# Performance work log

Hardware: AMD Instinct MI355X
Metric: run time of the kernel (lower is better)

The kernel has to match this reference:

```python
import jax, jax.numpy as jnp
import numpy as np

NUM_GROUPS = 32
EPS = 1e-6

def group_norm(x, gamma, beta):
    # x: (b, c, h, w)
    b, c, h, w = x.shape
    xg = x.reshape(b, NUM_GROUPS, c // NUM_GROUPS, h, w)
    mean = xg.mean(axis=(2, 3, 4), keepdims=True)
    var = xg.var(axis=(2, 3, 4), keepdims=True)
    xn = ((xg - mean) * jax.lax.rsqrt(var + EPS)).reshape(b, c, h, w)
    return xn * gamma[None, :, None, None] + beta[None, :, None, None]

def conv1x1(x, W, bias):
    # W: (out_c, in_c); 1x1 conv == channel matmul
    return jnp.einsum('oc,bchw->bohw', W, x) + bias[None, :, None, None]

def setup_inputs() -> dict:
    key = jax.random.key(0)
    ks = jax.random.split(key, 11)
    C = 512
    x = jax.random.normal(ks[0], (4, C, 64, 64), dtype=jnp.float32)
    s = 1.0 / np.sqrt(C)
    d = {
        'x': x,
        'gamma': jnp.ones((C,), jnp.float32),
        'beta': jnp.zeros((C,), jnp.float32),
        'Wq': jax.random.normal(ks[1], (C, C), jnp.float32) * s,
        'bq': jax.random.normal(ks[2], (C,), jnp.float32) * 0.01,
        'Wk': jax.random.normal(ks[3], (C, C), jnp.float32) * s,
        'bk': jax.random.normal(ks[4], (C,), jnp.float32) * 0.01,
        'Wv': jax.random.normal(ks[5], (C, C), jnp.float32) * s,
        'bv': jax.random.normal(ks[6], (C,), jnp.float32) * 0.01,
        'Wp': jax.random.normal(ks[7], (C, C), jnp.float32) * s,
        'bp': jax.random.normal(ks[8], (C,), jnp.float32) * 0.01,
    }
    return d

def reference(x, gamma, beta, Wq, bq, Wk, bk, Wv, bv, Wp, bp):
    b, c, h, w = x.shape
    hn = group_norm(x, gamma, beta)
    q = conv1x1(hn, Wq, bq).reshape(b, c, h * w)  # (b,c,n)
    k = conv1x1(hn, Wk, bk).reshape(b, c, h * w)
    v = conv1x1(hn, Wv, bv).reshape(b, c, h * w)
    scale = jnp.asarray(c, x.dtype) ** -0.5
    # scores[b,m,n] = sum_c q[b,c,m] * k[b,c,n]
    scores = jnp.einsum('bcm,bcn->bmn', q, k) * scale
    attn = jax.nn.softmax(scores, axis=2)  # softmax over key positions n
    # h_[b,c,m] = sum_n v[b,c,n] * attn[b,m,n]
    out = jnp.einsum('bcn,bmn->bcm', v, attn).reshape(b, c, h, w)
    return x + conv1x1(out, Wp, bp)
```

## Files before the change

### kernel.cpp

```cpp
#include <hip/hip_runtime.h>
#include <math.h>


#define BATCH 4
#define CH    512
#define NPOS  4096
#define NGRP  32
#define GSIZE (16 * NPOS)
#define WSZ   262144

typedef __attribute__((ext_vector_type(8))) short bf16x8;
typedef __attribute__((ext_vector_type(4))) float f32x4;

__device__ __forceinline__ ushort f2b(float x) {
    uint u = __float_as_uint(x);
    u += 0x7fff + ((u >> 16) & 1);
    return (ushort)(u >> 16);
}

__device__ __forceinline__ void gld16(void* lds, const void* g) {
    __builtin_amdgcn_global_load_lds(
        (const __attribute__((address_space(1))) void*)g,
        (__attribute__((address_space(3))) void*)lds, 16, 0, 0);
}

__global__ __launch_bounds__(256) void gn_stats_k(const float* __restrict__ x,
                                                  float* __restrict__ stats) {
    int bg = blockIdx.x;
    const float4* xp = reinterpret_cast<const float4*>(x + (size_t)bg * GSIZE);
    float s1 = 0.f, s2 = 0.f;
    for (int i = threadIdx.x; i < GSIZE / 4; i += 256) {
        float4 v = xp[i];
        s1 += v.x + v.y + v.z + v.w;
        s2 += v.x * v.x + v.y * v.y + v.z * v.z + v.w * v.w;
    }
    for (int off = 32; off > 0; off >>= 1) {
        s1 += __shfl_down(s1, off);
        s2 += __shfl_down(s2, off);
    }
    __shared__ float r1[4], r2[4];
    int wid = threadIdx.x >> 6;
    if ((threadIdx.x & 63) == 0) { r1[wid] = s1; r2[wid] = s2; }
    __syncthreads();
    if (threadIdx.x == 0) {
        float t1 = r1[0] + r1[1] + r1[2] + r1[3];
        float t2 = r2[0] + r2[1] + r2[2] + r2[3];
        float mean = t1 / (float)GSIZE;
        float var  = t2 / (float)GSIZE - mean * mean;
        stats[bg]       = mean;
        stats[128 + bg] = rsqrtf(var + 1e-6f);
    }
}

__global__ __launch_bounds__(256) void wcvt_k(
    const float* __restrict__ Wq, const float* __restrict__ Wk,
    const float* __restrict__ Wv, const float* __restrict__ Wp,
    ushort* __restrict__ W4) {
    int id = blockIdx.x;
    int sel = id >> 7, blk = id & 127;
    const float* src = sel == 0 ? Wq : (sel == 1 ? Wk : (sel == 2 ? Wv : Wp));
    const float4* s4 = (const float4*)(src + (size_t)blk * 2048);
    ushort4* d4 = (ushort4*)(W4 + (size_t)sel * WSZ + (size_t)blk * 2048);
    for (int i = threadIdx.x; i < 512; i += 256) {
        float4 v = s4[i];
        d4[i] = make_ushort4(f2b(v.x), f2b(v.y), f2b(v.z), f2b(v.w));
    }
}

__global__ __launch_bounds__(256) void hnT_k(
    const float* __restrict__ x, const float* __restrict__ gamma,
    const float* __restrict__ beta, const float* __restrict__ stats,
    ushort* __restrict__ hnT) {
    int bm = blockIdx.x * 64, c0 = blockIdx.y * 64, b = blockIdx.z;
    __shared__ ushort Ls[64][65];
    int t = threadIdx.x, tx = t & 15, ty = t >> 4;
    const float* xb = x + ((size_t)b * CH + c0) * NPOS + bm;
#pragma unroll
    for (int it = 0; it < 4; ++it) {
        int cc = ty + it * 16;
        int ch = c0 + cc;
        int bg = b * NGRP + (ch >> 4);
        float ga = stats[128 + bg] * gamma[ch];
        float be = beta[ch] - stats[bg] * ga;
        float4 v = *(const float4*)(xb + (size_t)cc * NPOS + tx * 4);
        Ls[cc][tx * 4 + 0] = f2b(v.x * ga + be);
        Ls[cc][tx * 4 + 1] = f2b(v.y * ga + be);
        Ls[cc][tx * 4 + 2] = f2b(v.z * ga + be);
        Ls[cc][tx * 4 + 3] = f2b(v.w * ga + be);
    }
    __syncthreads();
#pragma unroll
    for (int it = 0; it < 4; ++it) {
        int mm = ty + it * 16;
        ushort4 o;
        o.x = Ls[tx * 4 + 0][mm];
        o.y = Ls[tx * 4 + 1][mm];
        o.z = Ls[tx * 4 + 2][mm];
        o.w = Ls[tx * 4 + 3][mm];
        *(ushort4*)(hnT + ((size_t)(b * NPOS) + bm + mm) * CH + c0 + tx * 4) = o;
    }
}

__global__ __launch_bounds__(256) void qkv3_k(
    const ushort* __restrict__ hnT, const ushort* __restrict__ W4,
    const float* __restrict__ bq, const float* __restrict__ bk,
    const float* __restrict__ bv,
    ushort* __restrict__ qT, ushort* __restrict__ kT, ushort* __restrict__ vB) {
    int bm = blockIdx.x * 64, bo = blockIdx.y * 64, b = blockIdx.z;
    int t = threadIdx.x, l = t & 63, w = t >> 6;
    int wr = w & 1, wc = w >> 1;
    int lr = l & 15, lg = l >> 4;

    const ushort* ha  = hnT + ((size_t)(b * NPOS) + bm + wr * 32 + lr) * CH + lg * 8;
    const ushort* wqp = W4 + (size_t)(bo + wc * 32 + lr) * CH + lg * 8;
    const ushort* wkp = wqp + WSZ;
    const ushort* wvp = wkp + WSZ;

    f32x4 aq[2][2], ak[2][2], av[2][2];
#pragma unroll
    for (int i = 0; i < 2; ++i)
#pragma unroll
        for (int j = 0; j < 2; ++j) {
            aq[i][j] = (f32x4){0.f, 0.f, 0.f, 0.f};
            ak[i][j] = (f32x4){0.f, 0.f, 0.f, 0.f};
            av[i][j] = (f32x4){0.f, 0.f, 0.f, 0.f};
        }
#pragma unroll
    for (int c0 = 0; c0 < CH; c0 += 32) {
        bf16x8 a0 = *(const bf16x8*)(ha + c0);
        bf16x8 a1 = *(const bf16x8*)(ha + 16 * CH + c0);
        bf16x8 q0 = *(const bf16x8*)(wqp + c0);
        bf16x8 q1 = *(const bf16x8*)(wqp + 16 * CH + c0);
        bf16x8 k0 = *(const bf16x8*)(wkp + c0);
        bf16x8 k1 = *(const bf16x8*)(wkp + 16 * CH + c0);
        bf16x8 v0 = *(const bf16x8*)(wvp + c0);
        bf16x8 v1 = *(const bf16x8*)(wvp + 16 * CH + c0);
        aq[0][0] = __builtin_amdgcn_mfma_f32_16x16x32_bf16(a0, q0, aq[0][0], 0, 0, 0);
        aq[0][1] = __builtin_amdgcn_mfma_f32_16x16x32_bf16(a0, q1, aq[0][1], 0, 0, 0);
        aq[1][0] = __builtin_amdgcn_mfma_f32_16x16x32_bf16(a1, q0, aq[1][0], 0, 0, 0);
        aq[1][1] = __builtin_amdgcn_mfma_f32_16x16x32_bf16(a1, q1, aq[1][1], 0, 0, 0);
        ak[0][0] = __builtin_amdgcn_mfma_f32_16x16x32_bf16(a0, k0, ak[0][0], 0, 0, 0);
        ak[0][1] = __builtin_amdgcn_mfma_f32_16x16x32_bf16(a0, k1, ak[0][1], 0, 0, 0);
        ak[1][0] = __builtin_amdgcn_mfma_f32_16x16x32_bf16(a1, k0, ak[1][0], 0, 0, 0);
        ak[1][1] = __builtin_amdgcn_mfma_f32_16x16x32_bf16(a1, k1, ak[1][1], 0, 0, 0);
        av[0][0] = __builtin_amdgcn_mfma_f32_16x16x32_bf16(v0, a0, av[0][0], 0, 0, 0);
        av[0][1] = __builtin_amdgcn_mfma_f32_16x16x32_bf16(v0, a1, av[0][1], 0, 0, 0);
        av[1][0] = __builtin_amdgcn_mfma_f32_16x16x32_bf16(v1, a0, av[1][0], 0, 0, 0);
        av[1][1] = __builtin_amdgcn_mfma_f32_16x16x32_bf16(v1, a1, av[1][1], 0, 0, 0);
    }
    const float sc = 0.044194173824159216f;
#pragma unroll
    for (int j = 0; j < 2; ++j) {
        int o = bo + wc * 32 + j * 16 + lr;
        float bqv = bq[o], bkv = bk[o];
#pragma unroll
        for (int i = 0; i < 2; ++i)
#pragma unroll
            for (int r = 0; r < 4; ++r) {
                int m = bm + wr * 32 + i * 16 + 4 * lg + r;
                size_t base = ((size_t)(b * NPOS) + m) * CH + o;
                qT[base] = f2b((aq[i][j][r] + bqv) * sc);
                kT[base] = f2b(ak[i][j][r] + bkv);
            }
    }
#pragma unroll
    for (int i = 0; i < 2; ++i)
#pragma unroll
        for (int r = 0; r < 4; ++r) {
            int o = bo + wc * 32 + i * 16 + 4 * lg + r;
            float bvv = bv[o];
#pragma unroll
            for (int j = 0; j < 2; ++j) {
                int m = bm + wr * 32 + j * 16 + lr;
                vB[((size_t)(b * CH) + o) * NPOS + m] = f2b(av[i][j][r] + bvv);
            }
        }
}

__global__ __launch_bounds__(512) __attribute__((amdgpu_waves_per_eu(2, 2)))
void attn_k(
    const ushort* __restrict__ qT, const ushort* __restrict__ kT,
    const ushort* __restrict__ vB, ushort* __restrict__ aoT) {
    __shared__ ushort Ks[2][32 * 512];
    __shared__ ushort Vs[2][512 * 32];
    __shared__ ushort P_lds[64 * 40];
    __shared__ float mpart[2][4][16];

    int id = blockIdx.x;
    int b  = (id & 7) >> 1;
    int mt = ((id >> 3) << 1) | (id & 1);
    int m0 = mt * 64;

    int t = threadIdx.x, l = t & 63, w = t >> 6;
    int mi = w & 3, ci = w >> 2;
    int lr = l & 15, lg = l >> 4;

    const ushort* kTb = kT + (size_t)b * NPOS * CH;
    const ushort* vBb = vB + (size_t)b * CH * NPOS;

    auto stageK = [&](int n0, ushort* kbuf) {
#pragma unroll
        for (int i = 0; i < 4; ++i) {
            int n = w * 4 + i;
            const ushort* g = kTb + (size_t)(n0 + n) * CH + (l ^ (n & 7)) * 8;
            gld16(&kbuf[n * 512], g);
        }
    };
    auto stageV = [&](int n0, ushort* vbuf) {
#pragma unroll
        for (int i = 0; i < 4; ++i) {
            int cb = w * 64 + i * 16;
            int c  = cb + (l >> 2);
            int sc = (l & 3) ^ ((c >> 1) & 3);
            const ushort* g = vBb + (size_t)c * NPOS + n0 + sc * 8;
            gld16(&vbuf[cb * 32], g);
        }
    };

    stageK(0, &Ks[0][0]);
    stageV(0, &Vs[0][0]);

    const ushort* qrow = qT + ((size_t)(b * NPOS + m0 + mi * 16 + lr)) * CH + lg * 8;
    bf16x8 qf[16];
#pragma unroll
    for (int ks = 0; ks < 16; ++ks) qf[ks] = *(const bf16x8*)(qrow + ks * 32);

    f32x4 acc[16];
#pragma unroll
    for (int i = 0; i < 16; ++i) acc[i] = (f32x4){0.f, 0.f, 0.f, 0.f};
    float m_run[4], lsum[4];
#pragma unroll
    for (int r = 0; r < 4; ++r) { m_run[r] = -1e30f; lsum[r] = 0.f; }

    int zk = lr & 7;
    for (int nt = 0; nt < 128; ++nt) {
        const ushort* ks_cur = &Ks[nt & 1][0];
        const ushort* vs_cur = &Vs[nt & 1][0];
        asm volatile("s_waitcnt vmcnt(0)" ::: "memory");
        __builtin_amdgcn_s_barrier();
        __builtin_amdgcn_sched_barrier(0);
        if (nt + 1 < 128) {
            stageK((nt + 1) * 32, &Ks[(nt + 1) & 1][0]);
            stageV((nt + 1) * 32, &Vs[(nt + 1) & 1][0]);
        }
        f32x4 sp0 = {0.f, 0.f, 0.f, 0.f}, sp1 = sp0, sp2 = sp0, sp3 = sp0;
        const ushort* krow = &ks_cur[(ci * 16 + lr) * 512];
#pragma unroll
        for (int ks = 0; ks < 16; ks += 4) {
            bf16x8 kf0 = *(const bf16x8*)(krow + (((ks + 0) * 4 + lg) ^ zk) * 8);
            bf16x8 kf1 = *(const bf16x8*)(krow + (((ks + 1) * 4 + lg) ^ zk) * 8);
            bf16x8 kf2 = *(const bf16x8*)(krow + (((ks + 2) * 4 + lg) ^ zk) * 8);
            bf16x8 kf3 = *(const bf16x8*)(krow + (((ks + 3) * 4 + lg) ^ zk) * 8);
            sp0 = __builtin_amdgcn_mfma_f32_16x16x32_bf16(qf[ks + 0], kf0, sp0, 0, 0, 0);
            sp1 = __builtin_amdgcn_mfma_f32_16x16x32_bf16(qf[ks + 1], kf1, sp1, 0, 0, 0);
            sp2 = __builtin_amdgcn_mfma_f32_16x16x32_bf16(qf[ks + 2], kf2, sp2, 0, 0, 0);
            sp3 = __builtin_amdgcn_mfma_f32_16x16x32_bf16(qf[ks + 3], kf3, sp3, 0, 0, 0);
        }
        f32x4 s = (sp0 + sp1) + (sp2 + sp3);
        float pm[4];
#pragma unroll
        for (int r = 0; r < 4; ++r) pm[r] = s[r];
#pragma unroll
        for (int off = 1; off < 16; off <<= 1)
#pragma unroll
            for (int r = 0; r < 4; ++r) pm[r] = fmaxf(pm[r], __shfl_xor(pm[r], off));
        if (lr == 0) {
#pragma unroll
            for (int r = 0; r < 4; ++r) mpart[ci][mi][4 * lg + r] = pm[r];
        }
        asm volatile("s_waitcnt lgkmcnt(0)" ::: "memory");
        __builtin_amdgcn_s_barrier();
        __builtin_amdgcn_sched_barrier(0);
        float mt2[4];
        float growth = -1e30f;
#pragma unroll
        for (int r = 0; r < 4; ++r) {
            int row = 4 * lg + r;
            mt2[r] = fmaxf(mpart[0][mi][row], mpart[1][mi][row]);
            growth = fmaxf(growth, mt2[r] - m_run[r]);
        }
        bool resc = !__all(growth <= 8.0f);
        if (resc) {
            float alpha[4];
#pragma unroll
            for (int r = 0; r < 4; ++r) {
                float mnew = fmaxf(m_run[r], mt2[r]);
                alpha[r] = __expf(m_run[r] - mnew);
                m_run[r] = mnew;
                lsum[r] *= alpha[r];
            }
#pragma unroll
            for (int cs = 0; cs < 16; ++cs) {
                acc[cs][0] *= alpha[0]; acc[cs][1] *= alpha[1];
                acc[cs][2] *= alpha[2]; acc[cs][3] *= alpha[3];
            }
        }
        float p[4];
#pragma unroll
        for (int r = 0; r < 4; ++r) {
            p[r] = __expf(s[r] - m_run[r]);
            lsum[r] += p[r];
        }
#pragma unroll
        for (int r = 0; r < 4; ++r)
            P_lds[(mi * 16 + 4 * lg + r) * 40 + ci * 16 + lr] = f2b(p[r]);
        asm volatile("s_waitcnt lgkmcnt(0)" ::: "memory");
        __builtin_amdgcn_s_barrier();
        __builtin_amdgcn_sched_barrier(0);
        bf16x8 pa = *(const bf16x8*)&P_lds[(mi * 16 + lr) * 40 + lg * 8];
#pragma unroll
        for (int cs = 0; cs < 16; ++cs) {
            int c = ci * 256 + cs * 16 + lr;
            bf16x8 vf = *(const bf16x8*)&vs_cur[c * 32 + ((lg ^ ((c >> 1) & 3)) * 8)];
            acc[cs] = __builtin_amdgcn_mfma_f32_16x16x32_bf16(pa, vf, acc[cs], 0, 0, 0);
        }
    }
    float ls[4];
#pragma unroll
    for (int r = 0; r < 4; ++r) ls[r] = lsum[r];
#pragma unroll
    for (int off = 1; off < 16; off <<= 1)
#pragma unroll
        for (int r = 0; r < 4; ++r) ls[r] += __shfl_xor(ls[r], off);
    if (lr == 0) {
#pragma unroll
        for (int r = 0; r < 4; ++r) mpart[ci][mi][4 * lg + r] = ls[r];
    }
    asm volatile("s_waitcnt lgkmcnt(0)" ::: "memory");
    __builtin_amdgcn_s_barrier();
    __builtin_amdgcn_sched_barrier(0);
    float inv[4];
#pragma unroll
    for (int r = 0; r < 4; ++r) {
        int row = 4 * lg + r;
        inv[r] = 1.0f / (mpart[0][mi][row] + mpart[1][mi][row]);
    }
#pragma unroll
    for (int cs = 0; cs < 16; ++cs)
#pragma unroll
        for (int r = 0; r < 4; ++r)
            aoT[((size_t)(b * NPOS + m0 + mi * 16 + 4 * lg + r)) * CH
                + ci * 256 + cs * 16 + lr] = f2b(acc[cs][r] * inv[r]);
}

__global__ __launch_bounds__(256) void proj_k(
    const ushort* __restrict__ aoT, const ushort* __restrict__ W4,
    const float* __restrict__ bp, const float* __restrict__ x,
    float* __restrict__ out) {
    int bm = blockIdx.x * 64, bo = blockIdx.y * 64, b = blockIdx.z;
    int t = threadIdx.x, l = t & 63, w = t >> 6;
    int orh = w & 1, mc = w >> 1;
    int lr = l & 15, lg = l >> 4;

    const ushort* wp = W4 + 3 * (size_t)WSZ + (size_t)(bo + orh * 32 + lr) * CH + lg * 8;
    const ushort* ab = aoT + ((size_t)(b * NPOS) + bm + mc * 32 + lr) * CH + lg * 8;

    f32x4 ac[2][2];
#pragma unroll
    for (int i = 0; i < 2; ++i)
#pragma unroll
        for (int j = 0; j < 2; ++j) ac[i][j] = (f32x4){0.f, 0.f, 0.f, 0.f};
#pragma unroll
    for (int c0 = 0; c0 < CH; c0 += 32) {
        bf16x8 w0 = *(const bf16x8*)(wp + c0);
        bf16x8 w1 = *(const bf16x8*)(wp + 16 * CH + c0);
        bf16x8 b0 = *(const bf16x8*)(ab + c0);
        bf16x8 b1 = *(const bf16x8*)(ab + 16 * CH + c0);
        ac[0][0] = __builtin_amdgcn_mfma_f32_16x16x32_bf16(w0, b0, ac[0][0], 0, 0, 0);
        ac[0][1] = __builtin_amdgcn_mfma_f32_16x16x32_bf16(w0, b1, ac[0][1], 0, 0, 0);
        ac[1][0] = __builtin_amdgcn_mfma_f32_16x16x32_bf16(w1, b0, ac[1][0], 0, 0, 0);
        ac[1][1] = __builtin_amdgcn_mfma_f32_16x16x32_bf16(w1, b1, ac[1][1], 0, 0, 0);
    }
#pragma unroll
    for (int i = 0; i < 2; ++i)
#pragma unroll
        for (int r = 0; r < 4; ++r) {
            int o = bo + orh * 32 + i * 16 + 4 * lg + r;
            float bpv = bp[o];
#pragma unroll
            for (int j = 0; j < 2; ++j) {
                int m = bm + mc * 32 + j * 16 + lr;
                size_t base = ((size_t)(b * CH) + o) * NPOS + m;
                out[base] = ac[i][j][r] + bpv + x[base];
            }
        }
}

extern "C" void kernel_launch(void* const* d_in, const int* in_sizes, int n_in,
                              void* d_out, int out_size, void* d_ws, size_t ws_size,
                              hipStream_t stream) {
    const float* x     = (const float*)d_in[0];
    const float* gamma = (const float*)d_in[1];
    const float* beta  = (const float*)d_in[2];
    const float* Wq    = (const float*)d_in[3];
    const float* bq    = (const float*)d_in[4];
    const float* Wk    = (const float*)d_in[5];
    const float* bk    = (const float*)d_in[6];
    const float* Wv    = (const float*)d_in[7];
    const float* bv    = (const float*)d_in[8];
    const float* Wp    = (const float*)d_in[9];
    const float* bp    = (const float*)d_in[10];
    float* out = (float*)d_out;

    const size_t SZ = (size_t)BATCH * CH * NPOS;
    const size_t need = (5 * SZ + 4 * WSZ) * 2 + 1024;
    if (ws_size < need) return;

    ushort* qT  = (ushort*)d_ws;
    ushort* kT  = qT + SZ;
    ushort* vb  = kT + SZ;
    ushort* hnT = vb + SZ;
    ushort* aoT = hnT + SZ;
    ushort* W4  = aoT + SZ;
    float*  stats = (float*)(W4 + 4 * (size_t)WSZ);

    gn_stats_k<<<128, 256, 0, stream>>>(x, stats);
    wcvt_k<<<512, 256, 0, stream>>>(Wq, Wk, Wv, Wp, W4);
    hnT_k<<<dim3(64, 8, 4), 256, 0, stream>>>(x, gamma, beta, stats, hnT);
    qkv3_k<<<dim3(64, 8, 4), 256, 0, stream>>>(hnT, W4, bq, bk, bv, qT, kT, vb);
    attn_k<<<dim3(256), 512, 0, stream>>>(qT, kT, vb, aoT);
    proj_k<<<dim3(64, 8, 4), 256, 0, stream>>>(aoT, W4, bp, x, out);
}
```

Before: 500.1 us.

## Widen attention KV tile to 64 and single-buffer K/V with staggered prefetch

The attention kernel now processes 64 key positions per iteration instead of 32, halving the number of loop iterations and barriers, and drops double buffering. K and V each get a single LDS buffer. V for the current tile is loaded at the start of the iteration, while K for the next tile is issued after the max-reduction barrier, using partial vmcnt waits. The V swizzle is changed to an 8-way XOR. The aim is to amortize the softmax/barrier overhead over more MFMA work while keeping LDS use similar, at the risk of exposing V load latency before the PV matmul.

```diff
diff --git a/kernel.cpp b/kernel.cpp
--- a/kernel.cpp
+++ b/kernel.cpp
@@ -8,6 +8,8 @@
 #define NGRP  32
 #define GSIZE (16 * NPOS)
 #define WSZ   262144
+#define KVB   64
+#define NT    64
 
 typedef __attribute__((ext_vector_type(8))) short bf16x8;
 typedef __attribute__((ext_vector_type(4))) float f32x4;
@@ -181,9 +183,9 @@
 void attn_k(
     const ushort* __restrict__ qT, const ushort* __restrict__ kT,
     const ushort* __restrict__ vB, ushort* __restrict__ aoT) {
-    __shared__ ushort Ks[2][32 * 512];
-    __shared__ ushort Vs[2][512 * 32];
-    __shared__ ushort P_lds[64 * 40];
+    __shared__ ushort Ks[KVB * 512];
+    __shared__ ushort Vs[512 * KVB];
+    __shared__ ushort P_lds[64 * 72];
     __shared__ float mpart[2][4][16];
 
     int id = blockIdx.x;
@@ -198,27 +200,26 @@
     const ushort* kTb = kT + (size_t)b * NPOS * CH;
     const ushort* vBb = vB + (size_t)b * CH * NPOS;
 
-    auto stageK = [&](int n0, ushort* kbuf) {
-#pragma unroll
-        for (int i = 0; i < 4; ++i) {
-            int n = w * 4 + i;
+    auto stageK = [&](int n0) {
+#pragma unroll
+        for (int i = 0; i < 8; ++i) {
+            int n = w * 8 + i;
             const ushort* g = kTb + (size_t)(n0 + n) * CH + (l ^ (n & 7)) * 8;
-            gld16(&kbuf[n * 512], g);
+            gld16(&Ks[n * 512], g);
         }
     };
-    auto stageV = [&](int n0, ushort* vbuf) {
-#pragma unroll
-        for (int i = 0; i < 4; ++i) {
-            int cb = w * 64 + i * 16;
-            int c  = cb + (l >> 2);
-            int sc = (l & 3) ^ ((c >> 1) & 3);
+    auto stageV = [&](int n0) {
+#pragma unroll
+        for (int i = 0; i < 8; ++i) {
+            int cb = w * 64 + i * 8;
+            int c  = cb + (l >> 3);
+            int sc = (l & 7) ^ (c & 7);
             const ushort* g = vBb + (size_t)c * NPOS + n0 + sc * 8;
-            gld16(&vbuf[cb * 32], g);
+            gld16(&Vs[cb * KVB], g);
         }
     };
 
-    stageK(0, &Ks[0][0]);
-    stageV(0, &Vs[0][0]);
+    stageK(0);
 
     const ushort* qrow = qT + ((size_t)(b * NPOS + m0 + mi * 16 + lr)) * CH + lg * 8;
     bf16x8 qf[16];
@@ -233,33 +234,31 @@
     for (int r = 0; r < 4; ++r) { m_run[r] = -1e30f; lsum[r] = 0.f; }
 
     int zk = lr & 7;
-    for (int nt = 0; nt < 128; ++nt) {
-        const ushort* ks_cur = &Ks[nt & 1][0];
-        const ushort* vs_cur = &Vs[nt & 1][0];
+    for (int nt = 0; nt < NT; ++nt) {
+        int n0 = nt * KVB;
         asm volatile("s_waitcnt vmcnt(0)" ::: "memory");
         __builtin_amdgcn_s_barrier();
         __builtin_amdgcn_sched_barrier(0);
-        if (nt + 1 < 128) {
-            stageK((nt + 1) * 32, &Ks[(nt + 1) & 1][0]);
-            stageV((nt + 1) * 32, &Vs[(nt + 1) & 1][0]);
-        }
-        f32x4 sp0 = {0.f, 0.f, 0.f, 0.f}, sp1 = sp0, sp2 = sp0, sp3 = sp0;
-        const ushort* krow = &ks_cur[(ci * 16 + lr) * 512];
-#pragma unroll
-        for (int ks = 0; ks < 16; ks += 4) {
-            bf16x8 kf0 = *(const bf16x8*)(krow + (((ks + 0) * 4 + lg) ^ zk) * 8);
-            bf16x8 kf1 = *(const bf16x8*)(krow + (((ks + 1) * 4 + lg) ^ zk) * 8);
-            bf16x8 kf2 = *(const bf16x8*)(krow + (((ks + 2) * 4 + lg) ^ zk) * 8);
-            bf16x8 kf3 = *(const bf16x8*)(krow + (((ks + 3) * 4 + lg) ^ zk) * 8);
-            sp0 = __builtin_amdgcn_mfma_f32_16x16x32_bf16(qf[ks + 0], kf0, sp0, 0, 0, 0);
-            sp1 = __builtin_amdgcn_mfma_f32_16x16x32_bf16(qf[ks + 1], kf1, sp1, 0, 0, 0);
-            sp2 = __builtin_amdgcn_mfma_f32_16x16x32_bf16(qf[ks + 2], kf2, sp2, 0, 0, 0);
-            sp3 = __builtin_amdgcn_mfma_f32_16x16x32_bf16(qf[ks + 3], kf3, sp3, 0, 0, 0);
-        }
-        f32x4 s = (sp0 + sp1) + (sp2 + sp3);
+        stageV(n0);
+        f32x4 s0a = {0.f, 0.f, 0.f, 0.f}, s0b = s0a, s1a = s0a, s1b = s0a;
+        const ushort* krow0 = &Ks[(ci * 32 + lr) * 512];
+        const ushort* krow1 = &Ks[(ci * 32 + 16 + lr) * 512];
+#pragma unroll
+        for (int ks = 0; ks < 16; ks += 2) {
+            bf16x8 k0a = *(const bf16x8*)(krow0 + (((ks + 0) * 4 + lg) ^ zk) * 8);
+            bf16x8 k0b = *(const bf16x8*)(krow0 + (((ks + 1) * 4 + lg) ^ zk) * 8);
+            bf16x8 k1a = *(const bf16x8*)(krow1 + (((ks + 0) * 4 + lg) ^ zk) * 8);
+            bf16x8 k1b = *(const bf16x8*)(krow1 + (((ks + 1) * 4 + lg) ^ zk) * 8);
+            s0a = __builtin_amdgcn_mfma_f32_16x16x32_bf16(qf[ks + 0], k0a, s0a, 0, 0, 0);
+            s0b = __builtin_amdgcn_mfma_f32_16x16x32_bf16(qf[ks + 1], k0b, s0b, 0, 0, 0);
+            s1a = __builtin_amdgcn_mfma_f32_16x16x32_bf16(qf[ks + 0], k1a, s1a, 0, 0, 0);
+            s1b = __builtin_amdgcn_mfma_f32_16x16x32_bf16(qf[ks + 1], k1b, s1b, 0, 0, 0);
+        }
+        f32x4 s0 = s0a + s0b;
+        f32x4 s1 = s1a + s1b;
         float pm[4];
 #pragma unroll
-        for (int r = 0; r < 4; ++r) pm[r] = s[r];
+        for (int r = 0; r < 4; ++r) pm[r] = fmaxf(s0[r], s1[r]);
 #pragma unroll
         for (int off = 1; off < 16; off <<= 1)
 #pragma unroll
@@ -271,6 +270,7 @@
         asm volatile("s_waitcnt lgkmcnt(0)" ::: "memory");
         __builtin_amdgcn_s_barrier();
         __builtin_amdgcn_sched_barrier(0);
+        if (nt + 1 < NT) stageK((nt + 1) * KVB);
         float mt2[4];
         float growth = -1e30f;
 #pragma unroll
@@ -295,24 +295,36 @@
                 acc[cs][2] *= alpha[2]; acc[cs][3] *= alpha[3];
             }
         }
-        float p[4];
+        float p0[4], p1[4];
 #pragma unroll
         for (int r = 0; r < 4; ++r) {
-            p[r] = __expf(s[r] - m_run[r]);
-            lsum[r] += p[r];
-        }
-#pragma unroll
-        for (int r = 0; r < 4; ++r)
-            P_lds[(mi * 16 + 4 * lg + r) * 40 + ci * 16 + lr] = f2b(p[r]);
+            p0[r] = __expf(s0[r] - m_run[r]);
+            p1[r] = __expf(s1[r] - m_run[r]);
+            lsum[r] += p0[r] + p1[r];
+        }
+#pragma unroll
+        for (int r = 0; r < 4; ++r) {
+            int row = mi * 16 + 4 * lg + r;
+            P_lds[row * 72 + ci * 32 + lr]      = f2b(p0[r]);
+            P_lds[row * 72 + ci * 32 + 16 + lr] = f2b(p1[r]);
+        }
+        if (nt + 1 < NT) {
+            asm volatile("s_waitcnt vmcnt(8)" ::: "memory");
+        } else {
+            asm volatile("s_waitcnt vmcnt(0)" ::: "memory");
+        }
         asm volatile("s_waitcnt lgkmcnt(0)" ::: "memory");
         __builtin_amdgcn_s_barrier();
         __builtin_amdgcn_sched_barrier(0);
-        bf16x8 pa = *(const bf16x8*)&P_lds[(mi * 16 + lr) * 40 + lg * 8];
+        bf16x8 pa0 = *(const bf16x8*)&P_lds[(mi * 16 + lr) * 72 + lg * 8];
+        bf16x8 pa1 = *(const bf16x8*)&P_lds[(mi * 16 + lr) * 72 + 32 + lg * 8];
 #pragma unroll
         for (int cs = 0; cs < 16; ++cs) {
             int c = ci * 256 + cs * 16 + lr;
-            bf16x8 vf = *(const bf16x8*)&vs_cur[c * 32 + ((lg ^ ((c >> 1) & 3)) * 8)];
-            acc[cs] = __builtin_amdgcn_mfma_f32_16x16x32_bf16(pa, vf, acc[cs], 0, 0, 0);
+            bf16x8 vf0 = *(const bf16x8*)&Vs[c * KVB + (((0 * 4 + lg) ^ (c & 7)) * 8)];
+            bf16x8 vf1 = *(const bf16x8*)&Vs[c * KVB + (((1 * 4 + lg) ^ (c & 7)) * 8)];
+            acc[cs] = __builtin_amdgcn_mfma_f32_16x16x32_bf16(pa0, vf0, acc[cs], 0, 0, 0);
+            acc[cs] = __builtin_amdgcn_mfma_f32_16x16x32_bf16(pa1, vf1, acc[cs], 0, 0, 0);
         }
     }
     float ls[4];
```

Result: faster. 427.6 us (-14.5%).
